# Optimization experiments

Measured on AMD Instinct MI355X. Metric: run time of the kernel, lower is better.

The kernel has to match this reference:

```python
import jax, jax.numpy as jnp
import numpy as np

CH = [32, 64, 128, 256, 512]
# per decoder stage s (s=0 deepest): conv_a Cin = CH[3-s] + in_ch, Cout = CH[3-s]; conv_b CH[3-s]->CH[3-s]
STAGE_DIMS = [(768, 256), (384, 128), (192, 64), (96, 32)]


def three_interpolation(p1, p2, x2):
    """p1 [B,N1,3] dense coords, p2 [B,N2,3] sparse coords, x2 [B,C,N2] -> [B,C,N1]."""
    d2 = (jnp.sum(p1 * p1, -1)[:, :, None]
          - 2.0 * jnp.einsum('bnd,bmd->bnm', p1, p2)
          + jnp.sum(p2 * p2, -1)[:, None, :])            # [B,N1,N2] squared dists
    neg_d, idx = jax.lax.top_k(-d2, 3)                   # 3 nearest neighbors
    dist = jnp.maximum(-neg_d, 0.0)                      # [B,N1,3]
    w = 1.0 / (dist + 1e-8)
    w = w / jnp.sum(w, axis=-1, keepdims=True)           # inverse-distance weights
    gathered = jax.vmap(lambda x, i: x[:, i])(x2, idx)   # [B,C,N1,3]
    return jnp.einsum('bcnk,bnk->bcn', gathered, w)


def conv_bn_relu(x, W, g, b):
    # 1x1 conv1d + BN (eval: running mean 0, var 1) + ReLU
    y = jnp.einsum('oc,bcn->bon', W, x)
    return jax.nn.relu(y * g[None, :, None] + b[None, :, None])


def setup_inputs() -> dict:
    key = jax.random.key(0)
    B = 8
    Ns = [8192, 2048, 512, 128, 32]
    inp = {}
    keys = jax.random.split(key, 64)
    ki = 0
    for i, n in enumerate(Ns):
        inp[f'p{i}'] = jax.random.uniform(keys[ki], (B, n, 3), jnp.float32); ki += 1
        inp[f'f{i}'] = jax.random.normal(keys[ki], (B, CH[i], n), jnp.float32); ki += 1
    for s, (cin, cout) in enumerate(STAGE_DIMS):
        inp[f'w{s}a'] = jax.random.normal(keys[ki], (cout, cin), jnp.float32) * 0.05; ki += 1
        inp[f'g{s}a'] = 1.0 + 0.1 * jax.random.normal(keys[ki], (cout,), jnp.float32); ki += 1
        inp[f'b{s}a'] = 0.1 * jax.random.normal(keys[ki], (cout,), jnp.float32); ki += 1
        inp[f'w{s}b'] = jax.random.normal(keys[ki], (cout, cout), jnp.float32) * 0.05; ki += 1
        inp[f'g{s}b'] = 1.0 + 0.1 * jax.random.normal(keys[ki], (cout,), jnp.float32); ki += 1
        inp[f'b{s}b'] = 0.1 * jax.random.normal(keys[ki], (cout,), jnp.float32); ki += 1
    return inp


def reference(p0, p1, p2, p3, p4, f0, f1, f2, f3, f4,
              w0a, g0a, b0a, w0b, g0b, b0b,
              w1a, g1a, b1a, w1b, g1b, b1b,
              w2a, g2a, b2a, w2b, g2b, b2b,
              w3a, g3a, b3a, w3b, g3b, b3b):
    p = [p0, p1, p2, p3, p4]
    f = [f0, f1, f2, f3, f4]
    params = [(w0a, g0a, b0a, w0b, g0b, b0b),
              (w1a, g1a, b1a, w1b, g1b, b1b),
              (w2a, g2a, b2a, w2b, g2b, b2b),
              (w3a, g3a, b3a, w3b, g3b, b3b)]
    # decoder stage s propagates level (4-s) -> (3-s)
    for s in range(4):
        lvl = 3 - s
        interp = three_interpolation(p[lvl], p[lvl + 1], f[lvl + 1])
        x = jnp.concatenate([f[lvl], interp], axis=1)
        wa, ga, ba, wb, gb, bb = params[s]
        x = conv_bn_relu(x, wa, ga, ba)
        x = conv_bn_relu(x, wb, gb, bb)
        f[lvl] = x
    return f[0]
```

## Files before the change

kernel.cpp:

```cpp
#include <hip/hip_runtime.h>

#define KNN_INF 3.0e38f

struct KnnAll {
    const float* p1[4]; const float* p2[4];
    float* pd[4]; int* pi[4];
    int N1[4], N2[4], chunk[4], nchunk[4], nbx[4];
    int blkStart[4];
    int bs1, bs2, bs3;
};

__global__ void knn_all_kernel(KnnAll P) {
    __shared__ float4 sm4[256];
    int bid = blockIdx.x;
    int s = (bid >= P.bs1) + (bid >= P.bs2) + (bid >= P.bs3);
    int start = (s == 0) ? 0 : (s == 1) ? P.bs1 : (s == 2) ? P.bs2 : P.bs3;
    int local = bid - start;
    int nbx = P.nbx[s];
    int bx = local % nbx;
    int rest = local / nbx;
    int b = rest & 7;
    int z = rest >> 3;
    int N1 = P.N1[s], N2 = P.N2[s], chunk = P.chunk[s], nchunk = P.nchunk[s];
    int m0 = z * chunk;
    const float* p2b = P.p2[s] + ((size_t)b * N2 + m0) * 3;
    for (int m = threadIdx.x; m < chunk; m += blockDim.x) {
        float x = p2b[m * 3 + 0], y = p2b[m * 3 + 1], zz = p2b[m * 3 + 2];
        sm4[m] = make_float4(x, y, zz, x * x + y * y + zz * zz);
    }
    __syncthreads();
    int n = bx * blockDim.x + threadIdx.x;
    if (n >= N1) return;
    const float* p1b = P.p1[s] + ((size_t)b * N1 + n) * 3;
    float px = p1b[0], py = p1b[1], pz = p1b[2];
    float s1 = px * px + py * py + pz * pz;
    float d0 = KNN_INF, d1 = KNN_INF, d2 = KNN_INF;
    int i0 = 0, i1 = 0, i2 = 0;
    for (int m = 0; m < chunk; ++m) {
        float4 q = sm4[m];
        float dot = px * q.x + py * q.y + pz * q.z;
        float d = fmaf(-2.0f, dot, s1 + q.w);
        if (d < d2) {
            if (d < d1) {
                d2 = d1; i2 = i1;
                if (d < d0) { d1 = d0; i1 = i0; d0 = d; i0 = m; }
                else        { d1 = d;  i1 = m; }
            } else { d2 = d; i2 = m; }
        }
    }
    size_t base = (((size_t)b * N1 + n) * nchunk + z) * 3;
    float* pd = P.pd[s]; int* pi = P.pi[s];
    pd[base + 0] = d0; pd[base + 1] = d1; pd[base + 2] = d2;
    pi[base + 0] = m0 + i0; pi[base + 1] = m0 + i1; pi[base + 2] = m0 + i2;
}

struct MergeAll {
    const float* pd[4]; const int* pi[4];
    int* idx[4]; float* w[4];
    int nchunk[4], N1[4];
    int ts1, ts2, ts3;
};

__global__ void knn_merge_all_kernel(MergeAll P) {
    int t = blockIdx.x * blockDim.x + threadIdx.x;
    int s = (t >= P.ts1) + (t >= P.ts2) + (t >= P.ts3);
    int start = (s == 0) ? 0 : (s == 1) ? P.ts1 : (s == 2) ? P.ts2 : P.ts3;
    int lt = t - start;
    int nchunk = P.nchunk[s];
    float d0 = KNN_INF, d1 = KNN_INF, d2 = KNN_INF;
    int i0 = 0, i1 = 0, i2 = 0;
    const float* pd = P.pd[s]; const int* pi = P.pi[s];
    size_t base = (size_t)lt * nchunk * 3;
    for (int c = 0; c < nchunk * 3; ++c) {
        float d = pd[base + c];
        int   i = pi[base + c];
        if (d < d2) {
            if (d < d1) {
                d2 = d1; i2 = i1;
                if (d < d0) { d1 = d0; i1 = i0; d0 = d; i0 = i; }
                else        { d1 = d;  i1 = i; }
            } else { d2 = d; i2 = i; }
        }
    }
    float dd0 = fmaxf(d0, 0.0f), dd1 = fmaxf(d1, 0.0f), dd2 = fmaxf(d2, 0.0f);
    float w0 = 1.0f / (dd0 + 1e-8f);
    float w1 = 1.0f / (dd1 + 1e-8f);
    float w2 = 1.0f / (dd2 + 1e-8f);
    float wsum = w0 + w1 + w2;
    w0 /= wsum; w1 /= wsum; w2 /= wsum;
    size_t ob = (size_t)lt * 3;
    P.idx[s][ob + 0] = i0; P.idx[s][ob + 1] = i1; P.idx[s][ob + 2] = i2;
    P.w[s][ob + 0] = w0; P.w[s][ob + 1] = w1; P.w[s][ob + 2] = w2;
}

#define TO 32
#define TN 64
#define BK 16
template<bool PARTIAL>
__global__ __launch_bounds__(256) void conv_a_fused_kernel(
    const float* __restrict__ f1,
    const float* __restrict__ x2,
    const int*   __restrict__ idxS,
    const float* __restrict__ wS,
    const float* __restrict__ W,
    const float* __restrict__ g,
    const float* __restrict__ bv,
    float* __restrict__ Y,
    int C1, int C2, int N, int N2, int Cout, int chunk) {
    __shared__ float Ws[BK][TO];
    __shared__ float Xs[BK][TN];
    int Cin = C1 + C2;
    int zb = blockIdx.z;
    int b = zb & 7;
    int split = zb >> 3;
    int kBase = split * chunk;
    int oBase = blockIdx.y * TO;
    int nBase = blockIdx.x * TN;
    int tid = threadIdx.x;
    int tx = tid & 15;
    int ty = tid >> 4;
    int nn = tid & 63;
    int kk0 = tid >> 6;
    int n = nBase + nn;
    size_t gb = ((size_t)b * N + n) * 3;
    int j0 = idxS[gb + 0], j1 = idxS[gb + 1], j2 = idxS[gb + 2];
    float w0g = wS[gb + 0], w1g = wS[gb + 1], w2g = wS[gb + 2];
    const float* f1b = f1 + (size_t)b * C1 * N;
    const float* x2b = x2 + (size_t)b * C2 * N2;
    float acc[2][4] = {{0.f, 0.f, 0.f, 0.f}, {0.f, 0.f, 0.f, 0.f}};
    for (int k0 = kBase; k0 < kBase + chunk; k0 += BK) {
        for (int t = tid; t < TO * BK; t += 256) {
            int o = t / BK, kk = t % BK;
            Ws[kk][o] = W[(size_t)(oBase + o) * Cin + k0 + kk];
        }
#pragma unroll
        for (int i = 0; i < 4; ++i) {
            int kk = kk0 + i * 4;
            int k = k0 + kk;
            float v;
            if (k < C1) {
                v = f1b[(size_t)k * N + n];
            } else {
                const float* r = x2b + (size_t)(k - C1) * N2;
                v = r[j0] * w0g + r[j1] * w1g + r[j2] * w2g;
            }
            Xs[kk][nn] = v;
        }
        __syncthreads();
#pragma unroll
        for (int kk = 0; kk < BK; ++kk) {
            float w0 = Ws[kk][ty * 2 + 0];
            float w1 = Ws[kk][ty * 2 + 1];
            float4 xv = *reinterpret_cast<const float4*>(&Xs[kk][tx * 4]);
            acc[0][0] = fmaf(w0, xv.x, acc[0][0]);
            acc[0][1] = fmaf(w0, xv.y, acc[0][1]);
            acc[0][2] = fmaf(w0, xv.z, acc[0][2]);
            acc[0][3] = fmaf(w0, xv.w, acc[0][3]);
            acc[1][0] = fmaf(w1, xv.x, acc[1][0]);
            acc[1][1] = fmaf(w1, xv.y, acc[1][1]);
            acc[1][2] = fmaf(w1, xv.z, acc[1][2]);
            acc[1][3] = fmaf(w1, xv.w, acc[1][3]);
        }
        __syncthreads();
    }
#pragma unroll
    for (int r = 0; r < 2; ++r) {
        int o = oBase + ty * 2 + r;
        float4 st;
        if (PARTIAL) {
            st.x = acc[r][0]; st.y = acc[r][1]; st.z = acc[r][2]; st.w = acc[r][3];
            *reinterpret_cast<float4*>(&Y[((size_t)zb * Cout + o) * N + nBase + tx * 4]) = st;
        } else {
            float gg = g[o], bb = bv[o];
            st.x = fmaxf(fmaf(acc[r][0], gg, bb), 0.0f);
            st.y = fmaxf(fmaf(acc[r][1], gg, bb), 0.0f);
            st.z = fmaxf(fmaf(acc[r][2], gg, bb), 0.0f);
            st.w = fmaxf(fmaf(acc[r][3], gg, bb), 0.0f);
            *reinterpret_cast<float4*>(&Y[((size_t)b * Cout + o) * N + nBase + tx * 4]) = st;
        }
    }
}

template<bool PARTIAL>
__global__ __launch_bounds__(256) void conv_gemm_kernel(
    const float* __restrict__ X,
    const float* __restrict__ W,
    const float* __restrict__ g,
    const float* __restrict__ bv,
    float* __restrict__ Y,
    int Cin, int Cout, int N, int chunk) {
    __shared__ float Ws[BK][TO];
    __shared__ float Xs[BK][TN];
    int zb = blockIdx.z;
    int b = zb & 7;
    int split = zb >> 3;
    int kBase = split * chunk;
    int oBase = blockIdx.y * TO;
    int nBase = blockIdx.x * TN;
    int tid = threadIdx.x;
    int tx = tid & 15;
    int ty = tid >> 4;
    float acc[2][4] = {{0.f, 0.f, 0.f, 0.f}, {0.f, 0.f, 0.f, 0.f}};
    const float* Xb = X + (size_t)b * Cin * N;
    for (int k0 = kBase; k0 < kBase + chunk; k0 += BK) {
        for (int t = tid; t < TO * BK; t += 256) {
            int o = t / BK, kk = t % BK;
            Ws[kk][o] = W[(size_t)(oBase + o) * Cin + k0 + kk];
        }
        for (int t = tid; t < BK * TN; t += 256) {
            int kk = t / TN, nnn = t % TN;
            Xs[kk][nnn] = Xb[(size_t)(k0 + kk) * N + nBase + nnn];
        }
        __syncthreads();
#pragma unroll
        for (int kk = 0; kk < BK; ++kk) {
            float w0 = Ws[kk][ty * 2 + 0];
            float w1 = Ws[kk][ty * 2 + 1];
            float4 xv = *reinterpret_cast<const float4*>(&Xs[kk][tx * 4]);
            acc[0][0] = fmaf(w0, xv.x, acc[0][0]);
            acc[0][1] = fmaf(w0, xv.y, acc[0][1]);
            acc[0][2] = fmaf(w0, xv.z, acc[0][2]);
            acc[0][3] = fmaf(w0, xv.w, acc[0][3]);
            acc[1][0] = fmaf(w1, xv.x, acc[1][0]);
            acc[1][1] = fmaf(w1, xv.y, acc[1][1]);
            acc[1][2] = fmaf(w1, xv.z, acc[1][2]);
            acc[1][3] = fmaf(w1, xv.w, acc[1][3]);
        }
        __syncthreads();
    }
#pragma unroll
    for (int r = 0; r < 2; ++r) {
        int o = oBase + ty * 2 + r;
        float4 st;
        if (PARTIAL) {
            st.x = acc[r][0]; st.y = acc[r][1]; st.z = acc[r][2]; st.w = acc[r][3];
            *reinterpret_cast<float4*>(&Y[((size_t)zb * Cout + o) * N + nBase + tx * 4]) = st;
        } else {
            float gg = g[o], bb = bv[o];
            st.x = fmaxf(fmaf(acc[r][0], gg, bb), 0.0f);
            st.y = fmaxf(fmaf(acc[r][1], gg, bb), 0.0f);
            st.z = fmaxf(fmaf(acc[r][2], gg, bb), 0.0f);
            st.w = fmaxf(fmaf(acc[r][3], gg, bb), 0.0f);
            *reinterpret_cast<float4*>(&Y[((size_t)b * Cout + o) * N + nBase + tx * 4]) = st;
        }
    }
}

__global__ void reduce_bn_relu_kernel(const float* __restrict__ part,
                                      const float* __restrict__ g,
                                      const float* __restrict__ bv,
                                      float* __restrict__ Y,
                                      int Cout, int N, int total4, int nsplit, int stride4) {
    int t = blockIdx.x * blockDim.x + threadIdx.x;
    if (t >= total4) return;
    const float4* p4 = reinterpret_cast<const float4*>(part);
    float4 a = p4[t];
    for (int s = 1; s < nsplit; ++s) {
        float4 v = p4[t + (size_t)s * stride4];
        a.x += v.x; a.y += v.y; a.z += v.z; a.w += v.w;
    }
    int o = ((t * 4) / N) % Cout;
    float gg = g[o], bb = bv[o];
    float4 st;
    st.x = fmaxf(fmaf(a.x, gg, bb), 0.0f);
    st.y = fmaxf(fmaf(a.y, gg, bb), 0.0f);
    st.z = fmaxf(fmaf(a.z, gg, bb), 0.0f);
    st.w = fmaxf(fmaf(a.w, gg, bb), 0.0f);
    reinterpret_cast<float4*>(Y)[t] = st;
}

extern "C" void kernel_launch(void* const* d_in, const int* in_sizes, int n_in,
                              void* d_out, int out_size, void* d_ws, size_t ws_size,
                              hipStream_t stream) {
    const int B = 8;
    const int Ns[5]  = {8192, 2048, 512, 128, 32};
    const int CHs[5] = {32, 64, 128, 256, 512};

    const float* p[5];
    const float* f[5];
    for (int i = 0; i < 5; ++i) {
        p[i] = (const float*)d_in[2 * i];
        f[i] = (const float*)d_in[2 * i + 1];
    }

    int N1s[4], N2s[4], C1s[4], C2s[4];
    for (int s = 0; s < 4; ++s) {
        int lvl = 3 - s;
        N1s[s] = Ns[lvl]; N2s[s] = Ns[lvl + 1];
        C1s[s] = CHs[lvl];
        C2s[s] = (s == 0) ? CHs[4] : CHs[lvl + 1];
    }
    const int nchunks[4] = {1, 4, 8, 8};
    int chunks[4], nbxs[4];
    for (int s = 0; s < 4; ++s) {
        chunks[s] = N2s[s] / nchunks[s];
        nbxs[s] = (N1s[s] + 255) / 256;
    }

    float* ws = (float*)d_ws;
    int*   knn_idx = (int*)ws;
    float* knn_w   = ws + 262144;
    float* part_d  = ws + 524288;
    int*   part_i  = (int*)(ws + 2621440);
    float* bufA    = ws + 4718592;
    float* out0    = ws + 6815744;
    float* out1    = ws + 7077888;
    float* out2    = ws + 7602176;
    float* gpart   = ws + 8650752;
    float* outs[4] = {out0, out1, out2, (float*)d_out};

    int idxOff[4], pOff[4];
    {
        int a = 0, q = 0;
        for (int s = 0; s < 4; ++s) {
            idxOff[s] = a; a += B * N1s[s] * 3;
            pOff[s] = q;  q += B * N1s[s] * nchunks[s] * 3;
        }
    }

    KnnAll KP;
    int blk = 0;
    int bsArr[4];
    for (int s = 0; s < 4; ++s) {
        KP.p1[s] = p[3 - s]; KP.p2[s] = p[4 - s];
        KP.pd[s] = part_d + pOff[s]; KP.pi[s] = part_i + pOff[s];
        KP.N1[s] = N1s[s]; KP.N2[s] = N2s[s];
        KP.chunk[s] = chunks[s]; KP.nchunk[s] = nchunks[s]; KP.nbx[s] = nbxs[s];
        bsArr[s] = blk;
        blk += nbxs[s] * B * nchunks[s];
    }
    KP.bs1 = (blk, bsArr[1]); KP.bs2 = bsArr[2]; KP.bs3 = bsArr[3];
    knn_all_kernel<<<blk, 256, 0, stream>>>(KP);

    MergeAll MP;
    int tt = 0;
    int tsArr[4];
    for (int s = 0; s < 4; ++s) {
        MP.pd[s] = part_d + pOff[s]; MP.pi[s] = part_i + pOff[s];
        MP.idx[s] = knn_idx + idxOff[s]; MP.w[s] = knn_w + idxOff[s];
        MP.nchunk[s] = nchunks[s]; MP.N1[s] = N1s[s];
        tsArr[s] = tt;
        tt += B * N1s[s];
    }
    MP.ts1 = tsArr[1]; MP.ts2 = tsArr[2]; MP.ts3 = tsArr[3];
    knn_merge_all_kernel<<<(tt + 255) / 256, 256, 0, stream>>>(MP);

    const int nsA[4] = {6, 3, 2, 1};
    const int nsB[4] = {4, 2, 1, 1};

    for (int s = 0; s < 4; ++s) {
        int N1 = N1s[s], N2 = N2s[s];
        int C1 = C1s[s], C2 = C2s[s];
        int Cin = C1 + C2, Cout = C1;
        const float* x2 = (s == 0) ? f[4] : outs[s - 1];
        const float* wa = (const float*)d_in[10 + s * 6 + 0];
        const float* ga = (const float*)d_in[10 + s * 6 + 1];
        const float* ba = (const float*)d_in[10 + s * 6 + 2];
        const float* wb = (const float*)d_in[10 + s * 6 + 3];
        const float* gb = (const float*)d_in[10 + s * 6 + 4];
        const float* bb = (const float*)d_in[10 + s * 6 + 5];
        const int* idxS = knn_idx + idxOff[s];
        const float* wSb = knn_w + idxOff[s];

        {
            int nsplit = nsA[s];
            int chunk = Cin / nsplit;
            dim3 grid(N1 / TN, Cout / TO, B * nsplit);
            if (nsplit == 1) {
                conv_a_fused_kernel<false><<<grid, 256, 0, stream>>>(
                    f[3 - s], x2, idxS, wSb, wa, ga, ba, bufA, C1, C2, N1, N2, Cout, chunk);
            } else {
                conv_a_fused_kernel<true><<<grid, 256, 0, stream>>>(
                    f[3 - s], x2, idxS, wSb, wa, ga, ba, gpart, C1, C2, N1, N2, Cout, chunk);
                int total4 = B * Cout * N1 / 4;
                reduce_bn_relu_kernel<<<(total4 + 255) / 256, 256, 0, stream>>>(
                    gpart, ga, ba, bufA, Cout, N1, total4, nsplit, total4);
            }
        }
        {
            int nsplit = nsB[s];
            int chunk = Cout / nsplit;
            dim3 grid(N1 / TN, Cout / TO, B * nsplit);
            if (nsplit == 1) {
                conv_gemm_kernel<false><<<grid, 256, 0, stream>>>(
                    bufA, wb, gb, bb, outs[s], Cout, Cout, N1, chunk);
            } else {
                conv_gemm_kernel<true><<<grid, 256, 0, stream>>>(
                    bufA, wb, gb, bb, gpart, Cout, Cout, N1, chunk);
                int total4 = B * Cout * N1 / 4;
                reduce_bn_relu_kernel<<<(total4 + 255) / 256, 256, 0, stream>>>(
                    gpart, gb, bb, outs[s], Cout, N1, total4, nsplit, total4);
            }
        }
    }
}
```

Measured before the change: 231.5 us.

## Overlap largest-level KNN work with conv kernels of earlier decoder stages

Splits the KNN search for the largest level (8192 points against 2048) out of the upfront KNN kernel. Its blocks are appended as extra blocks to the conv_a, conv_b and reduce kernels of stages 0-2, so that work fills idle CUs while the small early-stage GEMMs run. The merge for that level is deferred until just before stage 3. The conv kernels now use a flattened 1D grid with a branch to the KNN body, and the extra shared memory may lower occupancy. Correctness depends on the hardcoded slice counts summing to the total number of KNN blocks.

```diff
diff --git a/kernel.cpp b/kernel.cpp
--- a/kernel.cpp
+++ b/kernel.cpp
@@ -1,37 +1,28 @@
 #include <hip/hip_runtime.h>
 
 #define KNN_INF 3.0e38f
-
-struct KnnAll {
-    const float* p1[4]; const float* p2[4];
-    float* pd[4]; int* pi[4];
-    int N1[4], N2[4], chunk[4], nchunk[4], nbx[4];
-    int blkStart[4];
-    int bs1, bs2, bs3;
-};
-
-__global__ void knn_all_kernel(KnnAll P) {
-    __shared__ float4 sm4[256];
-    int bid = blockIdx.x;
-    int s = (bid >= P.bs1) + (bid >= P.bs2) + (bid >= P.bs3);
-    int start = (s == 0) ? 0 : (s == 1) ? P.bs1 : (s == 2) ? P.bs2 : P.bs3;
-    int local = bid - start;
-    int nbx = P.nbx[s];
+#define TO 32
+#define TN 64
+#define BK 16
+
+__device__ __forceinline__ void knn_bu_body(
+    const float* __restrict__ p1, const float* __restrict__ p2,
+    float* __restrict__ pd, int* __restrict__ pi,
+    int N1, int N2, int chunk, int nchunk, int nbx, int local, float4* sm4) {
     int bx = local % nbx;
     int rest = local / nbx;
     int b = rest & 7;
     int z = rest >> 3;
-    int N1 = P.N1[s], N2 = P.N2[s], chunk = P.chunk[s], nchunk = P.nchunk[s];
     int m0 = z * chunk;
-    const float* p2b = P.p2[s] + ((size_t)b * N2 + m0) * 3;
-    for (int m = threadIdx.x; m < chunk; m += blockDim.x) {
+    const float* p2b = p2 + ((size_t)b * N2 + m0) * 3;
+    for (int m = threadIdx.x; m < chunk; m += 256) {
         float x = p2b[m * 3 + 0], y = p2b[m * 3 + 1], zz = p2b[m * 3 + 2];
         sm4[m] = make_float4(x, y, zz, x * x + y * y + zz * zz);
     }
     __syncthreads();
-    int n = bx * blockDim.x + threadIdx.x;
+    int n = bx * 256 + threadIdx.x;
     if (n >= N1) return;
-    const float* p1b = P.p1[s] + ((size_t)b * N1 + n) * 3;
+    const float* p1b = p1 + ((size_t)b * N1 + n) * 3;
     float px = p1b[0], py = p1b[1], pz = p1b[2];
     float s1 = px * px + py * py + pz * pz;
     float d0 = KNN_INF, d1 = KNN_INF, d2 = KNN_INF;
@@ -49,20 +40,40 @@
         }
     }
     size_t base = (((size_t)b * N1 + n) * nchunk + z) * 3;
-    float* pd = P.pd[s]; int* pi = P.pi[s];
     pd[base + 0] = d0; pd[base + 1] = d1; pd[base + 2] = d2;
     pi[base + 0] = m0 + i0; pi[base + 1] = m0 + i1; pi[base + 2] = m0 + i2;
+}
+
+struct KnnSlice {
+    const float* p1; const float* p2;
+    float* pd; int* pi;
+    int N1, N2, chunk, nchunk, nbx, buBase;
+};
+
+struct Knn3 {
+    const float* p1[3]; const float* p2[3];
+    float* pd[3]; int* pi[3];
+    int N1[3], N2[3], chunk[3], nchunk[3], nbx[3];
+    int bs1, bs2;
+};
+__global__ __launch_bounds__(256) void knn_small_kernel(Knn3 P) {
+    __shared__ float4 sm4[256];
+    int bid = blockIdx.x;
+    int s = (bid >= P.bs1) + (bid >= P.bs2);
+    int start = (s == 0) ? 0 : (s == 1) ? P.bs1 : P.bs2;
+    knn_bu_body(P.p1[s], P.p2[s], P.pd[s], P.pi[s], P.N1[s], P.N2[s],
+                P.chunk[s], P.nchunk[s], P.nbx[s], bid - start, sm4);
 }
 
 struct MergeAll {
     const float* pd[4]; const int* pi[4];
     int* idx[4]; float* w[4];
-    int nchunk[4], N1[4];
+    int nchunk[4];
     int ts1, ts2, ts3;
 };
-
-__global__ void knn_merge_all_kernel(MergeAll P) {
-    int t = blockIdx.x * blockDim.x + threadIdx.x;
+__global__ __launch_bounds__(256) void knn_merge_all_kernel(MergeAll P, int tbase, int tend) {
+    int t = tbase + blockIdx.x * 256 + threadIdx.x;
+    if (t >= tend) return;
     int s = (t >= P.ts1) + (t >= P.ts2) + (t >= P.ts3);
     int start = (s == 0) ? 0 : (s == 1) ? P.ts1 : (s == 2) ? P.ts2 : P.ts3;
     int lt = t - start;
@@ -93,29 +104,33 @@
     P.w[s][ob + 0] = w0; P.w[s][ob + 1] = w1; P.w[s][ob + 2] = w2;
 }
 
-#define TO 32
-#define TN 64
-#define BK 16
+
 template<bool PARTIAL>
-__global__ __launch_bounds__(256) void conv_a_fused_kernel(
-    const float* __restrict__ f1,
-    const float* __restrict__ x2,
-    const int*   __restrict__ idxS,
-    const float* __restrict__ wS,
-    const float* __restrict__ W,
-    const float* __restrict__ g,
-    const float* __restrict__ bv,
+__global__ __launch_bounds__(256) void conv_a_kernel(
+    const float* __restrict__ f1, const float* __restrict__ x2,
+    const int* __restrict__ idxS, const float* __restrict__ wS,
+    const float* __restrict__ W, const float* __restrict__ g, const float* __restrict__ bv,
     float* __restrict__ Y,
-    int C1, int C2, int N, int N2, int Cout, int chunk) {
+    int C1, int C2, int N, int N2, int Cout, int chunk,
+    int gx, int gy, int convTotal, KnnSlice S) {
     __shared__ float Ws[BK][TO];
     __shared__ float Xs[BK][TN];
+    __shared__ float4 sm4[256];
+    int bid = blockIdx.x;
+    if (bid >= convTotal) {
+        knn_bu_body(S.p1, S.p2, S.pd, S.pi, S.N1, S.N2, S.chunk, S.nchunk, S.nbx,
+                    S.buBase + (bid - convTotal), sm4);
+        return;
+    }
+    int bxx = bid % gx;
+    int byy = (bid / gx) % gy;
+    int zb  = bid / (gx * gy);
     int Cin = C1 + C2;
-    int zb = blockIdx.z;
     int b = zb & 7;
     int split = zb >> 3;
     int kBase = split * chunk;
-    int oBase = blockIdx.y * TO;
-    int nBase = blockIdx.x * TN;
+    int oBase = byy * TO;
+    int nBase = bxx * TN;
     int tid = threadIdx.x;
     int tx = tid & 15;
     int ty = tid >> 4;
@@ -182,21 +197,28 @@
 }
 
 template<bool PARTIAL>
-__global__ __launch_bounds__(256) void conv_gemm_kernel(
-    const float* __restrict__ X,
-    const float* __restrict__ W,
-    const float* __restrict__ g,
-    const float* __restrict__ bv,
-    float* __restrict__ Y,
-    int Cin, int Cout, int N, int chunk) {
+__global__ __launch_bounds__(256) void conv_b_kernel(
+    const float* __restrict__ X, const float* __restrict__ W,
+    const float* __restrict__ g, const float* __restrict__ bv,
+    float* __restrict__ Y, int Cin, int Cout, int N, int chunk,
+    int gx, int gy, int convTotal, KnnSlice S) {
     __shared__ float Ws[BK][TO];
     __shared__ float Xs[BK][TN];
-    int zb = blockIdx.z;
+    __shared__ float4 sm4[256];
+    int bid = blockIdx.x;
+    if (bid >= convTotal) {
+        knn_bu_body(S.p1, S.p2, S.pd, S.pi, S.N1, S.N2, S.chunk, S.nchunk, S.nbx,
+                    S.buBase + (bid - convTotal), sm4);
+        return;
+    }
+    int bxx = bid % gx;
+    int byy = (bid / gx) % gy;
+    int zb  = bid / (gx * gy);
     int b = zb & 7;
     int split = zb >> 3;
     int kBase = split * chunk;
-    int oBase = blockIdx.y * TO;
-    int nBase = blockIdx.x * TN;
+    int oBase = byy * TO;
+    int nBase = bxx * TN;
     int tid = threadIdx.x;
     int tx = tid & 15;
     int ty = tid >> 4;
@@ -246,12 +268,18 @@
     }
 }
 
-__global__ void reduce_bn_relu_kernel(const float* __restrict__ part,
-                                      const float* __restrict__ g,
-                                      const float* __restrict__ bv,
-                                      float* __restrict__ Y,
-                                      int Cout, int N, int total4, int nsplit, int stride4) {
-    int t = blockIdx.x * blockDim.x + threadIdx.x;
+__global__ __launch_bounds__(256) void reduce_bn_relu_kernel(
+    const float* __restrict__ part, const float* __restrict__ g, const float* __restrict__ bv,
+    float* __restrict__ Y, int Cout, int N, int total4, int nsplit, int stride4,
+    int convTotal, KnnSlice S) {
+    __shared__ float4 sm4[256];
+    int bid = blockIdx.x;
+    if (bid >= convTotal) {
+        knn_bu_body(S.p1, S.p2, S.pd, S.pi, S.N1, S.N2, S.chunk, S.nchunk, S.nbx,
+                    S.buBase + (bid - convTotal), sm4);
+        return;
+    }
+    int t = bid * 256 + threadIdx.x;
     if (t >= total4) return;
     const float4* p4 = reinterpret_cast<const float4*>(part);
     float4 a = p4[t];
@@ -318,10 +346,9 @@
         }
     }
 
-    KnnAll KP;
-    int blk = 0;
-    int bsArr[4];
-    for (int s = 0; s < 4; ++s) {
+    Knn3 KP;
+    int blk = 0, bsArr[3];
+    for (int s = 0; s < 3; ++s) {
         KP.p1[s] = p[3 - s]; KP.p2[s] = p[4 - s];
         KP.pd[s] = part_d + pOff[s]; KP.pi[s] = part_i + pOff[s];
         KP.N1[s] = N1s[s]; KP.N2[s] = N2s[s];
@@ -329,24 +356,37 @@
         bsArr[s] = blk;
         blk += nbxs[s] * B * nchunks[s];
     }
-    KP.bs1 = (blk, bsArr[1]); KP.bs2 = bsArr[2]; KP.bs3 = bsArr[3];
-    knn_all_kernel<<<blk, 256, 0, stream>>>(KP);
+    KP.bs1 = bsArr[1]; KP.bs2 = bsArr[2];
+    knn_small_kernel<<<blk, 256, 0, stream>>>(KP);
 
     MergeAll MP;
-    int tt = 0;
-    int tsArr[4];
+    int tt = 0, tsArr[4];
     for (int s = 0; s < 4; ++s) {
         MP.pd[s] = part_d + pOff[s]; MP.pi[s] = part_i + pOff[s];
         MP.idx[s] = knn_idx + idxOff[s]; MP.w[s] = knn_w + idxOff[s];
-        MP.nchunk[s] = nchunks[s]; MP.N1[s] = N1s[s];
+        MP.nchunk[s] = nchunks[s];
         tsArr[s] = tt;
         tt += B * N1s[s];
     }
     MP.ts1 = tsArr[1]; MP.ts2 = tsArr[2]; MP.ts3 = tsArr[3];
-    knn_merge_all_kernel<<<(tt + 255) / 256, 256, 0, stream>>>(MP);
+
+    knn_merge_all_kernel<<<(tsArr[3] + 255) / 256, 256, 0, stream>>>(MP, 0, tsArr[3]);
+
+    KnnSlice S3;
+    S3.p1 = p[0]; S3.p2 = p[1];
+    S3.pd = part_d + pOff[3]; S3.pi = part_i + pOff[3];
+    S3.N1 = N1s[3]; S3.N2 = N2s[3];
+    S3.chunk = chunks[3]; S3.nchunk = nchunks[3]; S3.nbx = nbxs[3];
+    S3.buBase = 0;
+    const int totalBu = nbxs[3] * B * nchunks[3];
+    int cur = 0;
 
     const int nsA[4] = {6, 3, 2, 1};
     const int nsB[4] = {4, 2, 1, 1};
+    const int sliceA[4]  = {192, 192, 256, 0};
+    const int sliceRA[4] = {128, 128, 256, 0};
+    const int sliceB[4]  = {192, 192, 256, 0};
+    const int sliceRB[4] = {128, 128, 0, 0};
 
     for (int s = 0; s < 4; ++s) {
         int N1 = N1s[s], N2 = N2s[s];
@@ -362,34 +402,56 @@
         const int* idxS = knn_idx + idxOff[s];
         const float* wSb = knn_w + idxOff[s];
 
+        if (s == 3) {
+            (void)totalBu;
+            knn_merge_all_kernel<<<(tt - tsArr[3] + 255) / 256, 256, 0, stream>>>(
+                MP, tsArr[3], tt);
+        }
+
         {
             int nsplit = nsA[s];
             int chunk = Cin / nsplit;
-            dim3 grid(N1 / TN, Cout / TO, B * nsplit);
+            int gx = N1 / TN, gy = Cout / TO, gz = B * nsplit;
+            int convTotal = gx * gy * gz;
+            KnnSlice S = S3; S.buBase = cur;
+            int cnt = sliceA[s]; cur += cnt;
             if (nsplit == 1) {
-                conv_a_fused_kernel<false><<<grid, 256, 0, stream>>>(
-                    f[3 - s], x2, idxS, wSb, wa, ga, ba, bufA, C1, C2, N1, N2, Cout, chunk);
+                conv_a_kernel<false><<<convTotal + cnt, 256, 0, stream>>>(
+                    f[3 - s], x2, idxS, wSb, wa, ga, ba, bufA,
+                    C1, C2, N1, N2, Cout, chunk, gx, gy, convTotal, S);
             } else {
-                conv_a_fused_kernel<true><<<grid, 256, 0, stream>>>(
-                    f[3 - s], x2, idxS, wSb, wa, ga, ba, gpart, C1, C2, N1, N2, Cout, chunk);
+                conv_a_kernel<true><<<convTotal + cnt, 256, 0, stream>>>(
+                    f[3 - s], x2, idxS, wSb, wa, ga, ba, gpart,
+                    C1, C2, N1, N2, Cout, chunk, gx, gy, convTotal, S);
                 int total4 = B * Cout * N1 / 4;
-                reduce_bn_relu_kernel<<<(total4 + 255) / 256, 256, 0, stream>>>(
-                    gpart, ga, ba, bufA, Cout, N1, total4, nsplit, total4);
+                int rb = (total4 + 255) / 256;
+                KnnSlice S2 = S3; S2.buBase = cur;
+                int cnt2 = sliceRA[s]; cur += cnt2;
+                reduce_bn_relu_kernel<<<rb + cnt2, 256, 0, stream>>>(
+                    gpart, ga, ba, bufA, Cout, N1, total4, nsplit, total4, rb, S2);
             }
         }
         {
             int nsplit = nsB[s];
             int chunk = Cout / nsplit;
-            dim3 grid(N1 / TN, Cout / TO, B * nsplit);
+            int gx = N1 / TN, gy = Cout / TO, gz = B * nsplit;
+            int convTotal = gx * gy * gz;
+            KnnSlice S = S3; S.buBase = cur;
+            int cnt = sliceB[s]; cur += cnt;
             if (nsplit == 1) {
-                conv_gemm_kernel<false><<<grid, 256, 0, stream>>>(
-                    bufA, wb, gb, bb, outs[s], Cout, Cout, N1, chunk);
+                conv_b_kernel<false><<<convTotal + cnt, 256, 0, stream>>>(
+                    bufA, wb, gb, bb, outs[s], Cout, Cout, N1, chunk,
+                    gx, gy, convTotal, S);
             } else {
-                conv_gemm_kernel<true><<<grid, 256, 0, stream>>>(
-                    bufA, wb, gb, bb, gpart, Cout, Cout, N1, chunk);
+                conv_b_kernel<true><<<convTotal + cnt, 256, 0, stream>>>(
+                    bufA, wb, gb, bb, gpart, Cout, Cout, N1, chunk,
+                    gx, gy, convTotal, S);
                 int total4 = B * Cout * N1 / 4;
-                reduce_bn_relu_kernel<<<(total4 + 255) / 256, 256, 0, stream>>>(
-                    gpart, gb, bb, outs[s], Cout, N1, total4, nsplit, total4);
+                int rb = (total4 + 255) / 256;
+                KnnSlice S2 = S3; S2.buBase = cur;
+                int cnt2 = sliceRB[s]; cur += cnt2;
+                reduce_bn_relu_kernel<<<rb + cnt2, 256, 0, stream>>>(
+                    gpart, gb, bb, outs[s], Cout, N1, total4, nsplit, total4, rb, S2);
             }
         }
     }
```

Measured after the change: 470.4 us. 103% more time.
